# Kernel tuning notes

Measured on AMD Instinct MI355X. Metric: run time of the kernel, lower is better.

Reference implementation:

```python
import jax, jax.numpy as jnp
import numpy as np

jax.config.update("jax_enable_x64", True)

ALPHA = 10.0
N_LAMBDA = 1.0
NON_REG = False


def setup_inputs() -> dict:
    key = jax.random.key(0)
    k1, k2 = jax.random.split(key)
    x = jax.random.normal(k1, (2, 3, 8192), dtype=jnp.float32)
    gt = jax.random.normal(k2, (2, 3, 8192), dtype=jnp.float32)
    return {"x": x, "gt": gt}


def _chamfer_raw(x, y):
    # x: [B, D, N], y: [B, D, M]; torch version upcasts to double
    x = x.astype(jnp.float64)
    y = y.astype(jnp.float64)
    xx = jnp.sum(x * x, axis=1)                      # [B, N]
    yy = jnp.sum(y * y, axis=1)                      # [B, M]
    zz = jnp.einsum("bdn,bdm->bnm", x, y)           # [B, N, M]
    P = xx[:, :, None] + yy[:, None, :] - 2.0 * zz   # squared L2 dists
    dist1 = jnp.min(P, axis=2)                       # [B, N] closest y for each x
    idx1 = jnp.argmin(P, axis=2)
    dist2 = jnp.min(P, axis=1)                       # [B, M] closest x for each y
    idx2 = jnp.argmin(P, axis=1)
    return dist1, dist2, idx1, idx2


def reference(x, gt):
    x = x.astype(jnp.float32)
    gt = gt.astype(jnp.float32)
    B, _, n_x = x.shape
    _, _, n_gt = gt.shape
    if NON_REG:
        frac_12 = max(1.0, n_x / n_gt)
        frac_21 = max(1.0, n_gt / n_x)
    else:
        frac_12 = n_x / n_gt
        frac_21 = n_gt / n_x

    dist1, dist2, idx1, idx2 = _chamfer_raw(x, gt)
    exp_dist1 = jnp.exp(-dist1 * ALPHA)
    exp_dist2 = jnp.exp(-dist2 * ALPHA)

    brow = jnp.arange(B)[:, None]
    # count1[b, j] = #x-points whose NN is gt point j
    count1 = jnp.zeros((B, n_gt), jnp.int64).at[brow, idx1].add(1)
    weight1 = count1[brow, idx1].astype(exp_dist1.dtype) ** N_LAMBDA
    weight1 = (1.0 / (weight1 + 1e-06)) * frac_21
    loss1 = jnp.mean(1.0 - exp_dist1 * weight1, axis=1)

    count2 = jnp.zeros((B, n_x), jnp.int64).at[brow, idx2].add(1)
    weight2 = count2[brow, idx2].astype(exp_dist2.dtype) ** N_LAMBDA
    weight2 = (1.0 / (weight2 + 1e-06)) * frac_12
    loss2 = jnp.mean(1.0 - exp_dist2 * weight2, axis=1)

    loss = (loss1 + loss2) / 2.0
    return jnp.mean(loss)
```

## Files before the change

### kernel.cpp

```cpp
#include <hip/hip_runtime.h>

#define BATCH   2
#define NPT     8192
#define THREADS 256
#define PPT     8
#define OWN     (THREADS * PPT)
#define OPP     128
#define NCI     (NPT / OWN)
#define NCJ     (NPT / OPP)
#define PGRID   (2 * BATCH * NCI * NCJ)
#define TOTAL   (2 * BATCH * NPT)
#define LGRID   64

typedef unsigned long long u64;

__global__ __launch_bounds__(THREADS) void dacd_pair_kernel(
    const float* __restrict__ x, const float* __restrict__ gt,
    u64* __restrict__ bestAll,
    float* __restrict__ S,
    unsigned* __restrict__ c,
    double* __restrict__ acc, unsigned* __restrict__ ticket)
{
    __shared__ float4 sg[OPP];

    const int t  = threadIdx.x;
    const int id = blockIdx.x;

    {
        const int z = id * 32 + (t & 31);
        if (t < 32)       S[z] = 0.0f;
        else if (t < 64)  c[z] = 0u;
        else if (id == 0 && t == 64) *acc = 0.0;
        else if (id == 0 && t == 65) *ticket = 0u;
    }

    const int dir = id & 1;
    const int b   = (id >> 1) & 1;
    const int ci  = (id >> 2) & (NCI - 1);
    const int cj  = id >> 4;

    const float* own = dir == 0 ? x : gt;
    const float* opp = dir == 0 ? gt : x;
    u64* best = bestAll + (size_t)dir * (BATCH * NPT) + (size_t)b * NPT;

    const float* ob = own + (size_t)b * (3 * NPT);
    const float* pb = opp + (size_t)b * (3 * NPT);

    if (t < OPP) {
        const int j = cj * OPP + t;
        const float gx = pb[j], gy = pb[NPT + j], gz = pb[2 * NPT + j];
        sg[t] = make_float4(-2.0f * gx, -2.0f * gy, -2.0f * gz,
                            fmaf(gx, gx, fmaf(gy, gy, gz * gz)));
    }

    float px[PPT], py[PPT], pz[PPT], bm[PPT];
    int   bj[PPT];
    const int i0 = ci * OWN + t;
    #pragma unroll
    for (int p = 0; p < PPT; ++p) {
        const int i = i0 + p * THREADS;
        px[p] = ob[i];
        py[p] = ob[NPT + i];
        pz[p] = ob[2 * NPT + i];
        bm[p] = INFINITY;
        bj[p] = 0;
    }
    __syncthreads();

    #pragma unroll 4
    for (int j = 0; j < OPP; ++j) {
        const float4 h = sg[j];
        #pragma unroll
        for (int p = 0; p < PPT; ++p) {
            const float m = fmaf(px[p], h.x,
                            fmaf(py[p], h.y,
                            fmaf(pz[p], h.z, h.w)));
            if (m < bm[p]) { bm[p] = m; bj[p] = j; }
        }
    }

    #pragma unroll
    for (int p = 0; p < PPT; ++p) {
        const float pp = fmaf(px[p], px[p], fmaf(py[p], py[p], pz[p] * pz[p]));
        const float d  = fmaxf(pp + bm[p], 0.0f);
        const u64 pk = ((u64)__float_as_uint(d) << 32)
                     | (unsigned)(cj * OPP + bj[p]);
        atomicMax(&best[i0 + p * THREADS], ~pk);
    }
}

__global__ __launch_bounds__(256) void dacd_hist_kernel(
    const u64* __restrict__ bestAll,
    float* __restrict__ S, unsigned* __restrict__ c)
{
    const int i = blockIdx.x * 256 + threadIdx.x;
    const u64 v = ~bestAll[i];
    const float d = __uint_as_float((unsigned)(v >> 32));
    const unsigned j = (unsigned)v & (NPT - 1);
    const int g = (i >> 13) << 13;
    const float e = __expf(-10.0f * d);
    atomicAdd(&S[g + j], e);
    atomicAdd(&c[g + j], 1u);
}

__global__ __launch_bounds__(256) void dacd_loss_kernel(
    const float* __restrict__ S, const unsigned* __restrict__ c,
    double* __restrict__ acc, unsigned* __restrict__ ticket,
    float* __restrict__ out)
{
    const int t = threadIdx.x;
    double local = 0.0;
    #pragma unroll
    for (int q = 0; q < 2; ++q) {
        const int j = blockIdx.x * 512 + q * 256 + t;
        local += (double)(S[j] / ((float)c[j] + 1e-6f));
    }
    #pragma unroll
    for (int off = 32; off > 0; off >>= 1)
        local += __shfl_down(local, off, 64);
    __shared__ double red[4];
    const int lane = t & 63, wid = t >> 6;
    if (lane == 0) red[wid] = local;
    __syncthreads();
    if (t == 0) {
        atomicAdd(acc, red[0] + red[1] + red[2] + red[3]);
        __threadfence();
        const unsigned old = atomicAdd(ticket, 1u);
        if (old == LGRID - 1) {
            const double T = atomicAdd(acc, 0.0);
            out[0] = (float)(((double)TOTAL - T) * (1.0 / (double)TOTAL));
        }
    }
}

extern "C" void kernel_launch(void* const* d_in, const int* in_sizes, int n_in,
                              void* d_out, int out_size, void* d_ws, size_t ws_size,
                              hipStream_t stream)
{
    const float* x  = (const float*)d_in[0];
    const float* gt = (const float*)d_in[1];
    float* out = (float*)d_out;

    u64* bestAll     = (u64*)d_ws;
    float* S         = (float*)(bestAll + TOTAL);
    unsigned* c      = (unsigned*)(S + TOTAL);
    double* acc      = (double*)(c + TOTAL);
    unsigned* ticket = (unsigned*)(acc + 1);

    dacd_pair_kernel<<<PGRID, THREADS, 0, stream>>>(x, gt, bestAll, S, c, acc, ticket);
    dacd_hist_kernel<<<TOTAL / 256, 256, 0, stream>>>(bestAll, S, c);
    dacd_loss_kernel<<<LGRID, 256, 0, stream>>>(S, c, acc, ticket, out);
}
```

Before: 94.21 us.

## Halve points per thread and fuse histogram and loss into one last-block kernel

The pair kernel now gives each thread 4 own points instead of 8. This doubles the grid and adds an occupancy hint, so more waves are spread across the CUs. The separate histogram and loss kernels become one kernel: each block does the scatter atomics, and the last block to take a ticket reduces all S/c entries through atomic reads. This removes one launch and the double accumulator, but the final reduction now runs serially in a single block, and each thread reuses its opposite-point tile over fewer own points.

```diff
diff --git a/kernel.cpp b/kernel.cpp
--- a/kernel.cpp
+++ b/kernel.cpp
@@ -3,23 +3,24 @@
 #define BATCH   2
 #define NPT     8192
 #define THREADS 256
-#define PPT     8
+#define PPT     4
 #define OWN     (THREADS * PPT)
 #define OPP     128
 #define NCI     (NPT / OWN)
 #define NCJ     (NPT / OPP)
 #define PGRID   (2 * BATCH * NCI * NCJ)
 #define TOTAL   (2 * BATCH * NPT)
-#define LGRID   64
+#define LTHREADS 512
+#define LGRID   (TOTAL / LTHREADS)
 
 typedef unsigned long long u64;
 
-__global__ __launch_bounds__(THREADS) void dacd_pair_kernel(
+__global__ __launch_bounds__(THREADS, 8) void dacd_pair_kernel(
     const float* __restrict__ x, const float* __restrict__ gt,
     u64* __restrict__ bestAll,
     float* __restrict__ S,
     unsigned* __restrict__ c,
-    double* __restrict__ acc, unsigned* __restrict__ ticket)
+    unsigned* __restrict__ ticket)
 {
     __shared__ float4 sg[OPP];
 
@@ -27,17 +28,16 @@
     const int id = blockIdx.x;
 
     {
-        const int z = id * 32 + (t & 31);
-        if (t < 32)       S[z] = 0.0f;
-        else if (t < 64)  c[z] = 0u;
-        else if (id == 0 && t == 64) *acc = 0.0;
-        else if (id == 0 && t == 65) *ticket = 0u;
+        const int z = id * 16 + (t & 15);
+        if (t < 16)       S[z] = 0.0f;
+        else if (t < 32)  c[z] = 0u;
+        else if (id == 0 && t == 32) *ticket = 0u;
     }
 
     const int dir = id & 1;
     const int b   = (id >> 1) & 1;
     const int ci  = (id >> 2) & (NCI - 1);
-    const int cj  = id >> 4;
+    const int cj  = id >> 5;
 
     const float* own = dir == 0 ? x : gt;
     const float* opp = dir == 0 ? gt : x;
@@ -89,47 +89,60 @@
     }
 }
 
-__global__ __launch_bounds__(256) void dacd_hist_kernel(
+__global__ __launch_bounds__(LTHREADS) void dacd_loss_kernel(
     const u64* __restrict__ bestAll,
-    float* __restrict__ S, unsigned* __restrict__ c)
-{
-    const int i = blockIdx.x * 256 + threadIdx.x;
-    const u64 v = ~bestAll[i];
-    const float d = __uint_as_float((unsigned)(v >> 32));
-    const unsigned j = (unsigned)v & (NPT - 1);
-    const int g = (i >> 13) << 13;
-    const float e = __expf(-10.0f * d);
-    atomicAdd(&S[g + j], e);
-    atomicAdd(&c[g + j], 1u);
-}
-
-__global__ __launch_bounds__(256) void dacd_loss_kernel(
-    const float* __restrict__ S, const unsigned* __restrict__ c,
-    double* __restrict__ acc, unsigned* __restrict__ ticket,
-    float* __restrict__ out)
+    float* __restrict__ S, unsigned* __restrict__ c,
+    unsigned* __restrict__ ticket, float* __restrict__ out)
 {
     const int t = threadIdx.x;
-    double local = 0.0;
-    #pragma unroll
-    for (int q = 0; q < 2; ++q) {
-        const int j = blockIdx.x * 512 + q * 256 + t;
-        local += (double)(S[j] / ((float)c[j] + 1e-6f));
+    const int i = blockIdx.x * LTHREADS + t;
+
+    {
+        const u64 v = ~bestAll[i];
+        const float d = __uint_as_float((unsigned)(v >> 32));
+        const unsigned j = (unsigned)v & (NPT - 1);
+        const int g = (i >> 13) << 13;
+        atomicAdd(&S[g + j], __expf(-10.0f * d));
+        atomicAdd(&c[g + j], 1u);
     }
+    __threadfence();
+    __syncthreads();
+
+    __shared__ bool lastBlk;
+    if (t == 0)
+        lastBlk = (atomicAdd(ticket, 1u) == LGRID - 1);
+    __syncthreads();
+    if (!lastBlk) return;
+
+    double s0 = 0.0, s1 = 0.0, s2 = 0.0, s3 = 0.0;
+    for (int k = t; k < TOTAL; k += LTHREADS * 4) {
+        const float a0 = atomicAdd(&S[k],                0.0f);
+        const float a1 = atomicAdd(&S[k + LTHREADS],     0.0f);
+        const float a2 = atomicAdd(&S[k + 2 * LTHREADS], 0.0f);
+        const float a3 = atomicAdd(&S[k + 3 * LTHREADS], 0.0f);
+        const unsigned b0 = atomicAdd(&c[k],                0u);
+        const unsigned b1 = atomicAdd(&c[k + LTHREADS],     0u);
+        const unsigned b2 = atomicAdd(&c[k + 2 * LTHREADS], 0u);
+        const unsigned b3 = atomicAdd(&c[k + 3 * LTHREADS], 0u);
+        s0 += (double)(a0 / ((float)b0 + 1e-6f));
+        s1 += (double)(a1 / ((float)b1 + 1e-6f));
+        s2 += (double)(a2 / ((float)b2 + 1e-6f));
+        s3 += (double)(a3 / ((float)b3 + 1e-6f));
+    }
+    double local = (s0 + s1) + (s2 + s3);
     #pragma unroll
     for (int off = 32; off > 0; off >>= 1)
         local += __shfl_down(local, off, 64);
-    __shared__ double red[4];
+
+    __shared__ double red[LTHREADS / 64];
     const int lane = t & 63, wid = t >> 6;
     if (lane == 0) red[wid] = local;
     __syncthreads();
     if (t == 0) {
-        atomicAdd(acc, red[0] + red[1] + red[2] + red[3]);
-        __threadfence();
-        const unsigned old = atomicAdd(ticket, 1u);
-        if (old == LGRID - 1) {
-            const double T = atomicAdd(acc, 0.0);
-            out[0] = (float)(((double)TOTAL - T) * (1.0 / (double)TOTAL));
-        }
+        double T = 0.0;
+        #pragma unroll
+        for (int w = 0; w < LTHREADS / 64; ++w) T += red[w];
+        out[0] = (float)(((double)TOTAL - T) * (1.0 / (double)TOTAL));
     }
 }
 
@@ -144,10 +157,8 @@
     u64* bestAll     = (u64*)d_ws;
     float* S         = (float*)(bestAll + TOTAL);
     unsigned* c      = (unsigned*)(S + TOTAL);
-    double* acc      = (double*)(c + TOTAL);
-    unsigned* ticket = (unsigned*)(acc + 1);
+    unsigned* ticket = (unsigned*)(c + TOTAL);
 
-    dacd_pair_kernel<<<PGRID, THREADS, 0, stream>>>(x, gt, bestAll, S, c, acc, ticket);
-    dacd_hist_kernel<<<TOTAL / 256, 256, 0, stream>>>(bestAll, S, c);
-    dacd_loss_kernel<<<LGRID, 256, 0, stream>>>(S, c, acc, ticket, out);
+    dacd_pair_kernel<<<PGRID, THREADS, 0, stream>>>(x, gt, bestAll, S, c, ticket);
+    dacd_loss_kernel<<<LGRID, LTHREADS, 0, stream>>>(bestAll, S, c, ticket, out);
 }
```

New measurement: 102.7 us. 1.09x slower.
